# Kernel optimization log

Measured on AMD Instinct MI355X. Metric: run time of the kernel, lower is better.

## Reference

```python
import jax, jax.numpy as jnp
import numpy as np

E = 64          # num_routed_experts
K = 6           # num_experts_per_token
NS = 2          # num_shared_experts
D = 512         # hidden_size
F = 512         # expert_intermediate_size = intermediate_size // 4


def setup_inputs() -> dict:
    key = jax.random.key(0)
    ks = jax.random.split(key, 8)
    s = 0.02
    return {
        "hidden_states": jax.random.normal(ks[0], (2, 1024, D), dtype=jnp.float32),
        "Wr": jax.random.normal(ks[1], (D, E), dtype=jnp.float32) * s,      # router
        "sWg": jax.random.normal(ks[2], (NS, D, F), dtype=jnp.float32) * s,  # shared gate_proj
        "sWu": jax.random.normal(ks[3], (NS, D, F), dtype=jnp.float32) * s,  # shared up_proj
        "sWd": jax.random.normal(ks[4], (NS, F, D), dtype=jnp.float32) * s,  # shared down_proj
        "Wg": jax.random.normal(ks[5], (E, D, F), dtype=jnp.float32) * s,    # routed gate_proj
        "Wu": jax.random.normal(ks[6], (E, D, F), dtype=jnp.float32) * s,    # routed up_proj
        "Wd": jax.random.normal(ks[7], (E, F, D), dtype=jnp.float32) * s,    # routed down_proj
    }


def _swiglu_ffn(x, wg, wu, wd):
    # x: (N, D); wg/wu: (D, F); wd: (F, D)
    return (jax.nn.silu(x @ wg) * (x @ wu)) @ wd


def reference(hidden_states, Wr, sWg, sWu, sWd, Wg, Wu, Wd):
    B, S, d = hidden_states.shape
    x = hidden_states.reshape(-1, d)  # (N, D)
    N = x.shape[0]

    # ---- shared experts (always on) ----
    shared = jnp.zeros_like(x)
    for e in range(NS):
        shared = shared + _swiglu_ffn(x, sWg[e], sWu[e], sWd[e])

    # ---- top-k router ----
    logits = x @ Wr                                   # (N, E)
    probs = jax.nn.softmax(logits, axis=-1)
    top_w, top_i = jax.lax.top_k(probs, K)            # (N, K)
    top_w = top_w / jnp.sum(top_w, axis=-1, keepdims=True)  # renormalize
    gate = jnp.zeros((N, E), dtype=x.dtype).at[jnp.arange(N)[:, None], top_i].set(top_w)

    # ---- routed experts: per-expert FFN, combined with sparse gate ----
    routed = jnp.zeros_like(x)
    for e in range(E):
        routed = routed + _swiglu_ffn(x, Wg[e], Wu[e], Wd[e]) * gate[:, e:e + 1]

    out = (shared + routed + x).reshape(B, S, d)
    return out
```

## Files before the change

kernel.cpp:

```cpp
#include <hip/hip_runtime.h>

#define N_TOK 2048
#define DD 512
#define FF 512
#define EE 64
#define TK 6
#define NG 66
#define RSLOT 12288
#define NSLOT 16384
#define BM 64
#define BN 64

typedef float f32x4 __attribute__((ext_vector_type(4)));
typedef __bf16 bf16x8 __attribute__((ext_vector_type(8)));
typedef short s16x8 __attribute__((ext_vector_type(8)));

__device__ __forceinline__ short f2bf(float f) {
  unsigned u = __builtin_bit_cast(unsigned, f);
  u = (u + 0x7fffu + ((u >> 16) & 1u)) >> 16;
  return (short)u;
}

__global__ void router_k(const float* __restrict__ x, const float* __restrict__ Wr,
                         int* __restrict__ top_i, float* __restrict__ top_w,
                         int* __restrict__ cnt) {
  int wave = threadIdx.x >> 6, lane = threadIdx.x & 63;
  int t0 = (blockIdx.x * 4 + wave) * 4;
  const float* x0 = x + (size_t)t0 * DD;
  float a0 = 0.f, a1 = 0.f, a2 = 0.f, a3 = 0.f;
  for (int k = 0; k < DD; ++k) {
    float wv = Wr[k * EE + lane];
    a0 = fmaf(x0[k], wv, a0);
    a1 = fmaf(x0[DD + k], wv, a1);
    a2 = fmaf(x0[2 * DD + k], wv, a2);
    a3 = fmaf(x0[3 * DD + k], wv, a3);
  }
  float accs[4] = {a0, a1, a2, a3};
#pragma unroll
  for (int tt = 0; tt < 4; ++tt) {
    int t = t0 + tt;
    float acc = accs[tt];
    float m = acc;
#pragma unroll
    for (int s = 32; s; s >>= 1) m = fmaxf(m, __shfl_xor(m, s));
    float p = __expf(acc - m);
    int wi[TK]; float wv[TK];
#pragma unroll
    for (int it = 0; it < TK; ++it) {
      float v = p;
#pragma unroll
      for (int s = 32; s; s >>= 1) v = fmaxf(v, __shfl_xor(v, s));
      unsigned long long b = __ballot(p == v);
      int idx = __ffsll((unsigned long long)b) - 1;
      wi[it] = idx; wv[it] = v;
      if (lane == idx) p = -1.f;
    }
    float wsum = 0.f;
#pragma unroll
    for (int it = 0; it < TK; ++it) wsum += wv[it];
    if (lane < TK) {
      int si = 0; float sv = 0.f;
#pragma unroll
      for (int it = 0; it < TK; ++it) if (lane == it) { si = wi[it]; sv = wv[it]; }
      top_i[t * TK + lane] = si;
      top_w[t * TK + lane] = sv / wsum;
      atomicAdd(&cnt[si], 1);
    }
  }
}

__global__ void offsets_k(const int* __restrict__ cnt, int* __restrict__ goff,
                          int* __restrict__ fill) {
  int i = threadIdx.x;
  if (i < EE) fill[i] = 0;
  if (i == 0) {
    int s = 0;
    for (int e = 0; e < EE; ++e) { goff[e] = s; s += cnt[e]; }
    goff[EE] = RSLOT;
    goff[EE + 1] = RSLOT + N_TOK;
    goff[EE + 2] = RSLOT + 2 * N_TOK;
  }
}

__global__ void scatter_k(const int* __restrict__ top_i, const float* __restrict__ top_w,
                          const int* __restrict__ goff, int* __restrict__ fill,
                          int* __restrict__ btok, float* __restrict__ bw) {
  int idx = blockIdx.x * blockDim.x + threadIdx.x;
  if (idx < RSLOT) {
    int e = top_i[idx];
    int pos = goff[e] + atomicAdd(&fill[e], 1);
    btok[pos] = idx / TK;
    bw[pos] = top_w[idx];
  } else if (idx < NSLOT) {
    int j = idx - RSLOT;
    btok[idx] = j & (N_TOK - 1);
    bw[idx] = 1.0f;
  }
}

__global__ void initout_k(const float* __restrict__ x, float* __restrict__ out, int n4) {
  int i = blockIdx.x * blockDim.x + threadIdx.x;
  if (i < n4) reinterpret_cast<f32x4*>(out)[i] = reinterpret_cast<const f32x4*>(x)[i];
}

__global__ __launch_bounds__(256) void gemm1_k(
    const float* __restrict__ x, const float* __restrict__ Wg, const float* __restrict__ Wu,
    const float* __restrict__ sWg, const float* __restrict__ sWu,
    const int* __restrict__ goff, const int* __restrict__ btok,
    short* __restrict__ H) {
  int g = blockIdx.z;
  int s0g = goff[g], cnt = goff[g + 1] - s0g;
  int mt = blockIdx.y;
  if (mt * BM >= cnt) return;
  int n0 = blockIdx.x * BN;
  const float* wgp = (g < EE) ? Wg + (size_t)g * DD * FF : sWg + (size_t)(g - EE) * DD * FF;
  const float* wup = (g < EE) ? Wu + (size_t)g * DD * FF : sWu + (size_t)(g - EE) * DD * FF;

  __shared__ short laA[4][BM][8];
  __shared__ short lbG[4][BN][8];
  __shared__ short lbU[4][BN][8];

  int tid = threadIdx.x;
  int lane = tid & 63;
  int w = tid >> 6;
  int wr = w >> 1, wc = w & 1;
  int lr = lane & 15, lgq = lane >> 4;

  int sm = tid >> 2, skb = tid & 3;
  int sn = tid & 63, skb2 = tid >> 6;

  int s0 = s0g + mt * BM;
  int tok = btok[((mt * BM + sm) < cnt) ? (s0 + sm) : s0];
  const float* xrow = x + (size_t)tok * DD;

  f32x4 accg[2][2], accu[2][2];
#pragma unroll
  for (int i = 0; i < 2; ++i)
#pragma unroll
    for (int j = 0; j < 2; ++j) {
      accg[i][j] = f32x4{0.f, 0.f, 0.f, 0.f};
      accu[i][j] = f32x4{0.f, 0.f, 0.f, 0.f};
    }

  for (int kt = 0; kt < DD / 32; ++kt) {
    int k0 = kt * 32;
    __syncthreads();
    {
      const float* p = xrow + k0 + skb * 8;
      f32x4 v0 = *reinterpret_cast<const f32x4*>(p);
      f32x4 v1 = *reinterpret_cast<const f32x4*>(p + 4);
      s16x8 o;
      o[0] = f2bf(v0[0]); o[1] = f2bf(v0[1]); o[2] = f2bf(v0[2]); o[3] = f2bf(v0[3]);
      o[4] = f2bf(v1[0]); o[5] = f2bf(v1[1]); o[6] = f2bf(v1[2]); o[7] = f2bf(v1[3]);
      *reinterpret_cast<s16x8*>(&laA[skb][sm][0]) = o;
    }
    {
      const float* bgp = wgp + (size_t)(k0 + skb2 * 8) * FF + n0 + sn;
      const float* bup = wup + (size_t)(k0 + skb2 * 8) * FF + n0 + sn;
      s16x8 og, ou;
#pragma unroll
      for (int i = 0; i < 8; ++i) {
        og[i] = f2bf(bgp[(size_t)i * FF]);
        ou[i] = f2bf(bup[(size_t)i * FF]);
      }
      *reinterpret_cast<s16x8*>(&lbG[skb2][sn][0]) = og;
      *reinterpret_cast<s16x8*>(&lbU[skb2][sn][0]) = ou;
    }
    __syncthreads();
    bf16x8 af[2], bgf[2], buf[2];
#pragma unroll
    for (int i = 0; i < 2; ++i)
      af[i] = *reinterpret_cast<const bf16x8*>(&laA[lgq][wr * 32 + i * 16 + lr][0]);
#pragma unroll
    for (int j = 0; j < 2; ++j) {
      bgf[j] = *reinterpret_cast<const bf16x8*>(&lbG[lgq][wc * 32 + j * 16 + lr][0]);
      buf[j] = *reinterpret_cast<const bf16x8*>(&lbU[lgq][wc * 32 + j * 16 + lr][0]);
    }
#pragma unroll
    for (int i = 0; i < 2; ++i)
#pragma unroll
      for (int j = 0; j < 2; ++j) {
        accg[i][j] = __builtin_amdgcn_mfma_f32_16x16x32_bf16(af[i], bgf[j], accg[i][j], 0, 0, 0);
        accu[i][j] = __builtin_amdgcn_mfma_f32_16x16x32_bf16(af[i], buf[j], accu[i][j], 0, 0, 0);
      }
  }
#pragma unroll
  for (int i = 0; i < 2; ++i)
#pragma unroll
    for (int j = 0; j < 2; ++j)
#pragma unroll
      for (int r = 0; r < 4; ++r) {
        int mrow = wr * 32 + i * 16 + lgq * 4 + r;
        if (mt * BM + mrow < cnt) {
          float gg = accg[i][j][r];
          float uu = accu[i][j][r];
          float hv = (gg / (1.f + __expf(-gg))) * uu;
          int col = n0 + wc * 32 + j * 16 + lr;
          H[(size_t)(s0 + mrow) * FF + col] = f2bf(hv);
        }
      }
}

__global__ __launch_bounds__(256) void gemm2_k(
    const short* __restrict__ H, const float* __restrict__ Wd, const float* __restrict__ sWd,
    const int* __restrict__ goff, const int* __restrict__ btok, const float* __restrict__ bw,
    float* __restrict__ out) {
  int g = blockIdx.z;
  int s0g = goff[g], cnt = goff[g + 1] - s0g;
  int mt = blockIdx.y;
  if (mt * BM >= cnt) return;
  int n0 = blockIdx.x * BN;
  const float* wdp = (g < EE) ? Wd + (size_t)g * FF * DD : sWd + (size_t)(g - EE) * FF * DD;

  __shared__ short laA[4][BM][8];
  __shared__ short lbB[4][BN][8];

  int tid = threadIdx.x;
  int lane = tid & 63;
  int w = tid >> 6;
  int wr = w >> 1, wc = w & 1;
  int lr = lane & 15, lgq = lane >> 4;

  int sm = tid >> 2, skb = tid & 3;
  int sn = tid & 63, skb2 = tid >> 6;

  int s0 = s0g + mt * BM;
  int srow = s0 + sm;
  if (srow > NSLOT - 1) srow = NSLOT - 1;
  const short* hrow = H + (size_t)srow * FF;

  f32x4 acc[2][2];
#pragma unroll
  for (int i = 0; i < 2; ++i)
#pragma unroll
    for (int j = 0; j < 2; ++j) acc[i][j] = f32x4{0.f, 0.f, 0.f, 0.f};

  for (int kt = 0; kt < FF / 32; ++kt) {
    int k0 = kt * 32;
    __syncthreads();
    {
      s16x8 v = *reinterpret_cast<const s16x8*>(hrow + k0 + skb * 8);
      *reinterpret_cast<s16x8*>(&laA[skb][sm][0]) = v;
    }
    {
      const float* bp = wdp + (size_t)(k0 + skb2 * 8) * DD + n0 + sn;
      s16x8 ob;
#pragma unroll
      for (int i = 0; i < 8; ++i) ob[i] = f2bf(bp[(size_t)i * DD]);
      *reinterpret_cast<s16x8*>(&lbB[skb2][sn][0]) = ob;
    }
    __syncthreads();
    bf16x8 af[2], bf[2];
#pragma unroll
    for (int i = 0; i < 2; ++i)
      af[i] = *reinterpret_cast<const bf16x8*>(&laA[lgq][wr * 32 + i * 16 + lr][0]);
#pragma unroll
    for (int j = 0; j < 2; ++j)
      bf[j] = *reinterpret_cast<const bf16x8*>(&lbB[lgq][wc * 32 + j * 16 + lr][0]);
#pragma unroll
    for (int i = 0; i < 2; ++i)
#pragma unroll
      for (int j = 0; j < 2; ++j)
        acc[i][j] = __builtin_amdgcn_mfma_f32_16x16x32_bf16(af[i], bf[j], acc[i][j], 0, 0, 0);
  }
#pragma unroll
  for (int i = 0; i < 2; ++i)
#pragma unroll
    for (int j = 0; j < 2; ++j)
#pragma unroll
      for (int r = 0; r < 4; ++r) {
        int mrow = wr * 32 + i * 16 + lgq * 4 + r;
        if (mt * BM + mrow < cnt) {
          int slot = s0 + mrow;
          int tok = btok[slot];
          float wv = bw[slot];
          int col = n0 + wc * 32 + j * 16 + lr;
          atomicAdd(&out[(size_t)tok * DD + col], acc[i][j][r] * wv);
        }
      }
}

extern "C" void kernel_launch(void* const* d_in, const int* in_sizes, int n_in,
                              void* d_out, int out_size, void* d_ws, size_t ws_size,
                              hipStream_t stream) {
  const float* x   = (const float*)d_in[0];
  const float* Wr  = (const float*)d_in[1];
  const float* sWg = (const float*)d_in[2];
  const float* sWu = (const float*)d_in[3];
  const float* sWd = (const float*)d_in[4];
  const float* Wg  = (const float*)d_in[5];
  const float* Wu  = (const float*)d_in[6];
  const float* Wd  = (const float*)d_in[7];
  float* out = (float*)d_out;

  char* wsb = (char*)d_ws;
  size_t off = 0;
  short* H = (short*)(wsb + off);    off += (size_t)NSLOT * FF * 2;
  int*   top_i = (int*)(wsb + off);  off += (size_t)RSLOT * 4;
  float* top_w = (float*)(wsb + off); off += (size_t)RSLOT * 4;
  int*   btok = (int*)(wsb + off);   off += (size_t)NSLOT * 4;
  float* bwt  = (float*)(wsb + off); off += (size_t)NSLOT * 4;
  int*   cnt  = (int*)(wsb + off);   off += 256;
  int*   fill = (int*)(wsb + off);   off += 256;
  int*   goff = (int*)(wsb + off);   off += 256;

  hipMemsetAsync(cnt, 0, 256, stream);
  router_k<<<N_TOK / 16, 256, 0, stream>>>(x, Wr, top_i, top_w, cnt);
  offsets_k<<<1, 64, 0, stream>>>(cnt, goff, fill);
  scatter_k<<<NSLOT / 256, 256, 0, stream>>>(top_i, top_w, goff, fill, btok, bwt);
  int n4 = out_size / 4;
  initout_k<<<(n4 + 255) / 256, 256, 0, stream>>>(x, out, n4);
  dim3 grid1(FF / BN, N_TOK / BM, NG);
  gemm1_k<<<grid1, 256, 0, stream>>>(x, Wg, Wu, sWg, sWu, goff, btok, H);
  dim3 grid2(DD / BN, N_TOK / BM, NG);
  gemm2_k<<<grid2, 256, 0, stream>>>(H, Wd, sWd, goff, btok, bwt, out);
}
```

Before: 211.3 us.

## Pipeline MoE GEMMs with async global-to-LDS loads and compact tile worklist

Measured after the change: 196.9 us. -6.8%, faster.

```diff
diff --git a/kernel.cpp b/kernel.cpp
--- a/kernel.cpp
+++ b/kernel.cpp
@@ -10,40 +10,75 @@
 #define NSLOT 16384
 #define BM 64
 #define BN 64
+#define NT 16
+#define MAXT 320
 
 typedef float f32x4 __attribute__((ext_vector_type(4)));
 typedef __bf16 bf16x8 __attribute__((ext_vector_type(8)));
-typedef short s16x8 __attribute__((ext_vector_type(8)));
-
-__device__ __forceinline__ short f2bf(float f) {
-  unsigned u = __builtin_bit_cast(unsigned, f);
-  u = (u + 0x7fffu + ((u >> 16) & 1u)) >> 16;
-  return (short)u;
-}
-
-__global__ void router_k(const float* __restrict__ x, const float* __restrict__ Wr,
-                         int* __restrict__ top_i, float* __restrict__ top_w,
-                         int* __restrict__ cnt) {
-  int wave = threadIdx.x >> 6, lane = threadIdx.x & 63;
-  int t0 = (blockIdx.x * 4 + wave) * 4;
-  const float* x0 = x + (size_t)t0 * DD;
-  float a0 = 0.f, a1 = 0.f, a2 = 0.f, a3 = 0.f;
-  for (int k = 0; k < DD; ++k) {
-    float wv = Wr[k * EE + lane];
-    a0 = fmaf(x0[k], wv, a0);
-    a1 = fmaf(x0[DD + k], wv, a1);
-    a2 = fmaf(x0[2 * DD + k], wv, a2);
-    a3 = fmaf(x0[3 * DD + k], wv, a3);
-  }
-  float accs[4] = {a0, a1, a2, a3};
+
+__device__ __forceinline__ unsigned cvtpk(float lo, float hi) {
+  unsigned r;
+  asm("v_cvt_pk_bf16_f32 %0, %1, %2" : "=v"(r) : "v"(lo), "v"(hi));
+  return r;
+}
+
+__device__ __forceinline__ bf16x8 pack8(f32x4 a, f32x4 b) {
+  union { unsigned u[4]; bf16x8 v; } r;
+  r.u[0] = cvtpk(a[0], a[1]); r.u[1] = cvtpk(a[2], a[3]);
+  r.u[2] = cvtpk(b[0], b[1]); r.u[3] = cvtpk(b[2], b[3]);
+  return r.v;
+}
+
+__device__ __forceinline__ void gll16(const void* g, void* l) {
+  __builtin_amdgcn_global_load_lds(
+      (const __attribute__((address_space(1))) unsigned int*)g,
+      (__attribute__((address_space(3))) unsigned int*)l, 16, 0, 0);
+}
+
+__global__ __launch_bounds__(256) void router_k(
+    const float* __restrict__ x, const float* __restrict__ Wr,
+    int* __restrict__ top_i, float* __restrict__ top_w, int* __restrict__ cnt) {
+  __shared__ float xs[16 * 512];
+  __shared__ float part[4][16][64];
+  int tid = threadIdx.x, lane = tid & 63, w = tid >> 6;
+  int t0 = blockIdx.x * 16;
+
+  const f32x4* xin = (const f32x4*)(x + (size_t)t0 * DD);
+  f32x4* xs4 = (f32x4*)xs;
+#pragma unroll
+  for (int i = 0; i < 8; ++i) xs4[i * 256 + tid] = xin[i * 256 + tid];
+  __syncthreads();
+
+  float acc[16];
+#pragma unroll
+  for (int t = 0; t < 16; ++t) acc[t] = 0.f;
+  for (int kk = 0; kk < 32; ++kk) {
+    int k = w * 128 + kk * 4;
+    float w0 = Wr[(size_t)(k + 0) * EE + lane];
+    float w1 = Wr[(size_t)(k + 1) * EE + lane];
+    float w2 = Wr[(size_t)(k + 2) * EE + lane];
+    float w3 = Wr[(size_t)(k + 3) * EE + lane];
+#pragma unroll
+    for (int t = 0; t < 16; ++t) {
+      f32x4 xv = *(const f32x4*)&xs[t * 512 + k];
+      acc[t] = fmaf(xv[0], w0, acc[t]);
+      acc[t] = fmaf(xv[1], w1, acc[t]);
+      acc[t] = fmaf(xv[2], w2, acc[t]);
+      acc[t] = fmaf(xv[3], w3, acc[t]);
+    }
+  }
+#pragma unroll
+  for (int t = 0; t < 16; ++t) part[w][t][lane] = acc[t];
+  __syncthreads();
+
 #pragma unroll
   for (int tt = 0; tt < 4; ++tt) {
-    int t = t0 + tt;
-    float acc = accs[tt];
-    float m = acc;
+    int t = w * 4 + tt;
+    float l0 = part[0][t][lane] + part[1][t][lane] + part[2][t][lane] + part[3][t][lane];
+    float m = l0;
 #pragma unroll
     for (int s = 32; s; s >>= 1) m = fmaxf(m, __shfl_xor(m, s));
-    float p = __expf(acc - m);
+    float p = __expf(l0 - m);
     int wi[TK]; float wv[TK];
 #pragma unroll
     for (int it = 0; it < TK; ++it) {
@@ -58,28 +93,43 @@
     float wsum = 0.f;
 #pragma unroll
     for (int it = 0; it < TK; ++it) wsum += wv[it];
+    int tg = t0 + t;
     if (lane < TK) {
       int si = 0; float sv = 0.f;
 #pragma unroll
       for (int it = 0; it < TK; ++it) if (lane == it) { si = wi[it]; sv = wv[it]; }
-      top_i[t * TK + lane] = si;
-      top_w[t * TK + lane] = sv / wsum;
+      top_i[tg * TK + lane] = si;
+      top_w[tg * TK + lane] = sv / wsum;
       atomicAdd(&cnt[si], 1);
     }
   }
 }
 
 __global__ void offsets_k(const int* __restrict__ cnt, int* __restrict__ goff,
-                          int* __restrict__ fill) {
+                          int* __restrict__ fill, int* __restrict__ wk_g,
+                          int* __restrict__ wk_mt, int* __restrict__ nitems) {
   int i = threadIdx.x;
-  if (i < EE) fill[i] = 0;
-  if (i == 0) {
-    int s = 0;
-    for (int e = 0; e < EE; ++e) { goff[e] = s; s += cnt[e]; }
+  fill[i] = 0;
+  int c = cnt[i];
+  int s = c;
+#pragma unroll
+  for (int d = 1; d < 64; d <<= 1) { int t = __shfl_up(s, d); if (i >= d) s += t; }
+  goff[i] = s - c;
+  if (i == 63) {
     goff[EE] = RSLOT;
     goff[EE + 1] = RSLOT + N_TOK;
     goff[EE + 2] = RSLOT + 2 * N_TOK;
   }
+  int nt = (c + BM - 1) >> 6;
+  int ts = nt;
+#pragma unroll
+  for (int d = 1; d < 64; d <<= 1) { int t = __shfl_up(ts, d); if (i >= d) ts += t; }
+  int texcl = ts - nt;
+  for (int t = 0; t < nt; ++t) { wk_g[texcl + t] = i; wk_mt[texcl + t] = t; }
+  int tot = __shfl(ts, 63);
+  wk_g[tot + i] = EE + (i >> 5);
+  wk_mt[tot + i] = i & 31;
+  if (i == 0) nitems[0] = tot + 64;
 }
 
 __global__ void scatter_k(const int* __restrict__ top_i, const float* __restrict__ top_w,
@@ -107,31 +157,51 @@
     const float* __restrict__ x, const float* __restrict__ Wg, const float* __restrict__ Wu,
     const float* __restrict__ sWg, const float* __restrict__ sWu,
     const int* __restrict__ goff, const int* __restrict__ btok,
+    const int* __restrict__ wk_g, const int* __restrict__ wk_mt,
+    const int* __restrict__ nitems,
     short* __restrict__ H) {
-  int g = blockIdx.z;
+  int item = blockIdx.y;
+  if (item >= nitems[0]) return;
+  int g = wk_g[item], mt = wk_mt[item];
   int s0g = goff[g], cnt = goff[g + 1] - s0g;
-  int mt = blockIdx.y;
-  if (mt * BM >= cnt) return;
   int n0 = blockIdx.x * BN;
   const float* wgp = (g < EE) ? Wg + (size_t)g * DD * FF : sWg + (size_t)(g - EE) * DD * FF;
   const float* wup = (g < EE) ? Wu + (size_t)g * DD * FF : sWu + (size_t)(g - EE) * DD * FF;
 
-  __shared__ short laA[4][BM][8];
-  __shared__ short lbG[4][BN][8];
-  __shared__ short lbU[4][BN][8];
+  __shared__ __align__(16) float lds[2][6144];
 
   int tid = threadIdx.x;
   int lane = tid & 63;
   int w = tid >> 6;
   int wr = w >> 1, wc = w & 1;
   int lr = lane & 15, lgq = lane >> 4;
-
-  int sm = tid >> 2, skb = tid & 3;
-  int sn = tid & 63, skb2 = tid >> 6;
-
   int s0 = s0g + mt * BM;
-  int tok = btok[((mt * BM + sm) < cnt) ? (s0 + sm) : s0];
-  const float* xrow = x + (size_t)tok * DD;
+
+  const float* sp[6];
+  int ldsoff[6], strf[6];
+#pragma unroll
+  for (int q = 0; q < 6; ++q) {
+    int c = w * 6 + q;
+    ldsoff[q] = c * 256;
+    if (c < 8) {
+      int row = c * 8 + (lane >> 3);
+      int tok = btok[s0 + row];
+      sp[q] = x + (size_t)tok * DD + (((lane & 7) ^ (lane >> 3)) << 2);
+      strf[q] = 32;
+    } else if (c < 16) {
+      int cc = c - 8;
+      int krow = cc * 4 + (lane >> 4);
+      int colf = ((((lane & 15) << 4) ^ (((cc >> 1) & 3) << 5)) >> 2);
+      sp[q] = wgp + (size_t)krow * FF + n0 + colf;
+      strf[q] = 32 * FF;
+    } else {
+      int cc = c - 16;
+      int krow = cc * 4 + (lane >> 4);
+      int colf = ((((lane & 15) << 4) ^ (((cc >> 1) & 3) << 5)) >> 2);
+      sp[q] = wup + (size_t)krow * FF + n0 + colf;
+      strf[q] = 32 * FF;
+    }
+  }
 
   f32x4 accg[2][2], accu[2][2];
 #pragma unroll
@@ -142,48 +212,60 @@
       accu[i][j] = f32x4{0.f, 0.f, 0.f, 0.f};
     }
 
-  for (int kt = 0; kt < DD / 32; ++kt) {
-    int k0 = kt * 32;
+  auto STAGE = [&](int b, int kt) {
+#pragma unroll
+    for (int q = 0; q < 6; ++q)
+      gll16(sp[q] + (size_t)kt * strf[q], &lds[b][ldsoff[q]]);
+  };
+  auto COMPUTE = [&](int b) {
+    const float* Am = &lds[b][0];
+    const float* Gm = &lds[b][2048];
+    const float* Um = &lds[b][4096];
+    bf16x8 af[2], bg[2], bu[2];
+#pragma unroll
+    for (int i = 0; i < 2; ++i) {
+      int row = wr * 32 + i * 16 + lr;
+      int sw = (row & 7) << 2;
+      f32x4 v0 = *(const f32x4*)&Am[row * 32 + ((lgq * 8) ^ sw)];
+      f32x4 v1 = *(const f32x4*)&Am[row * 32 + ((lgq * 8 + 4) ^ sw)];
+      af[i] = pack8(v0, v1);
+    }
+#pragma unroll
+    for (int j = 0; j < 2; ++j) {
+      int col = wc * 32 + j * 16 + lr;
+      int cx = col ^ (lgq << 3);
+      int kb = lgq * 8;
+      f32x4 g0, g1, u0, u1;
+#pragma unroll
+      for (int i2 = 0; i2 < 4; ++i2) {
+        g0[i2] = Gm[(kb + i2) * 64 + cx];
+        g1[i2] = Gm[(kb + 4 + i2) * 64 + cx];
+        u0[i2] = Um[(kb + i2) * 64 + cx];
+        u1[i2] = Um[(kb + 4 + i2) * 64 + cx];
+      }
+      bg[j] = pack8(g0, g1);
+      bu[j] = pack8(u0, u1);
+    }
+#pragma unroll
+    for (int i = 0; i < 2; ++i)
+#pragma unroll
+      for (int j = 0; j < 2; ++j) {
+        accg[i][j] = __builtin_amdgcn_mfma_f32_16x16x32_bf16(af[i], bg[j], accg[i][j], 0, 0, 0);
+        accu[i][j] = __builtin_amdgcn_mfma_f32_16x16x32_bf16(af[i], bu[j], accu[i][j], 0, 0, 0);
+      }
+  };
+
+  STAGE(0, 0);
+  __syncthreads();
+  int b = 0;
+#pragma unroll 1
+  for (int kt = 0; kt < NT; ++kt) {
+    if (kt + 1 < NT) STAGE(b ^ 1, kt + 1);
+    COMPUTE(b);
     __syncthreads();
-    {
-      const float* p = xrow + k0 + skb * 8;
-      f32x4 v0 = *reinterpret_cast<const f32x4*>(p);
-      f32x4 v1 = *reinterpret_cast<const f32x4*>(p + 4);
-      s16x8 o;
-      o[0] = f2bf(v0[0]); o[1] = f2bf(v0[1]); o[2] = f2bf(v0[2]); o[3] = f2bf(v0[3]);
-      o[4] = f2bf(v1[0]); o[5] = f2bf(v1[1]); o[6] = f2bf(v1[2]); o[7] = f2bf(v1[3]);
-      *reinterpret_cast<s16x8*>(&laA[skb][sm][0]) = o;
-    }
-    {
-      const float* bgp = wgp + (size_t)(k0 + skb2 * 8) * FF + n0 + sn;
-      const float* bup = wup + (size_t)(k0 + skb2 * 8) * FF + n0 + sn;
-      s16x8 og, ou;
-#pragma unroll
-      for (int i = 0; i < 8; ++i) {
-        og[i] = f2bf(bgp[(size_t)i * FF]);
-        ou[i] = f2bf(bup[(size_t)i * FF]);
-      }
-      *reinterpret_cast<s16x8*>(&lbG[skb2][sn][0]) = og;
-      *reinterpret_cast<s16x8*>(&lbU[skb2][sn][0]) = ou;
-    }
-    __syncthreads();
-    bf16x8 af[2], bgf[2], buf[2];
-#pragma unroll
-    for (int i = 0; i < 2; ++i)
-      af[i] = *reinterpret_cast<const bf16x8*>(&laA[lgq][wr * 32 + i * 16 + lr][0]);
-#pragma unroll
-    for (int j = 0; j < 2; ++j) {
-      bgf[j] = *reinterpret_cast<const bf16x8*>(&lbG[lgq][wc * 32 + j * 16 + lr][0]);
-      buf[j] = *reinterpret_cast<const bf16x8*>(&lbU[lgq][wc * 32 + j * 16 + lr][0]);
-    }
-#pragma unroll
-    for (int i = 0; i < 2; ++i)
-#pragma unroll
-      for (int j = 0; j < 2; ++j) {
-        accg[i][j] = __builtin_amdgcn_mfma_f32_16x16x32_bf16(af[i], bgf[j], accg[i][j], 0, 0, 0);
-        accu[i][j] = __builtin_amdgcn_mfma_f32_16x16x32_bf16(af[i], buf[j], accu[i][j], 0, 0, 0);
-      }
-  }
+    b ^= 1;
+  }
+
 #pragma unroll
   for (int i = 0; i < 2; ++i)
 #pragma unroll
@@ -196,7 +278,7 @@
           float uu = accu[i][j][r];
           float hv = (gg / (1.f + __expf(-gg))) * uu;
           int col = n0 + wc * 32 + j * 16 + lr;
-          H[(size_t)(s0 + mrow) * FF + col] = f2bf(hv);
+          H[(size_t)(s0 + mrow) * FF + col] = (short)(cvtpk(hv, hv) & 0xffffu);
         }
       }
 }
@@ -204,30 +286,44 @@
 __global__ __launch_bounds__(256) void gemm2_k(
     const short* __restrict__ H, const float* __restrict__ Wd, const float* __restrict__ sWd,
     const int* __restrict__ goff, const int* __restrict__ btok, const float* __restrict__ bw,
+    const int* __restrict__ wk_g, const int* __restrict__ wk_mt,
+    const int* __restrict__ nitems,
     float* __restrict__ out) {
-  int g = blockIdx.z;
+  int item = blockIdx.y;
+  if (item >= nitems[0]) return;
+  int g = wk_g[item], mt = wk_mt[item];
   int s0g = goff[g], cnt = goff[g + 1] - s0g;
-  int mt = blockIdx.y;
-  if (mt * BM >= cnt) return;
   int n0 = blockIdx.x * BN;
   const float* wdp = (g < EE) ? Wd + (size_t)g * FF * DD : sWd + (size_t)(g - EE) * FF * DD;
 
-  __shared__ short laA[4][BM][8];
-  __shared__ short lbB[4][BN][8];
+  __shared__ __align__(16) short lds[2][6144];
 
   int tid = threadIdx.x;
   int lane = tid & 63;
   int w = tid >> 6;
   int wr = w >> 1, wc = w & 1;
   int lr = lane & 15, lgq = lane >> 4;
-
-  int sm = tid >> 2, skb = tid & 3;
-  int sn = tid & 63, skb2 = tid >> 6;
-
   int s0 = s0g + mt * BM;
-  int srow = s0 + sm;
-  if (srow > NSLOT - 1) srow = NSLOT - 1;
-  const short* hrow = H + (size_t)srow * FF;
+
+  const char* sp[3];
+  int ldsbyte[3], strb[3];
+#pragma unroll
+  for (int q = 0; q < 3; ++q) {
+    int c = w * 3 + q;
+    ldsbyte[q] = c * 1024;
+    if (c < 4) {
+      int row = c * 16 + (lane >> 2);
+      int slot = s0 + row;
+      sp[q] = (const char*)(H + (size_t)slot * FF + (((lane & 3) ^ ((lane >> 2) & 3)) << 3));
+      strb[q] = 64;
+    } else {
+      int cc = c - 4;
+      int krow = cc * 4 + (lane >> 4);
+      int colf = ((((lane & 15) << 4) ^ (((cc >> 1) & 3) << 5)) >> 2);
+      sp[q] = (const char*)(wdp + (size_t)krow * DD + n0 + colf);
+      strb[q] = 32 * DD * 4;
+    }
+  }
 
   f32x4 acc[2][2];
 #pragma unroll
@@ -235,49 +331,67 @@
 #pragma unroll
     for (int j = 0; j < 2; ++j) acc[i][j] = f32x4{0.f, 0.f, 0.f, 0.f};
 
-  for (int kt = 0; kt < FF / 32; ++kt) {
-    int k0 = kt * 32;
+  auto STAGE = [&](int b, int kt) {
+#pragma unroll
+    for (int q = 0; q < 3; ++q)
+      gll16(sp[q] + (size_t)kt * strb[q], (char*)lds[b] + ldsbyte[q]);
+  };
+  auto COMPUTE = [&](int b) {
+    const short* Hm = lds[b];
+    const float* Bm = (const float*)(lds[b] + 2048);
+    bf16x8 af[2], bd[2];
+#pragma unroll
+    for (int i = 0; i < 2; ++i) {
+      int row = wr * 32 + i * 16 + lr;
+      af[i] = *(const bf16x8*)&Hm[row * 32 + ((lgq * 8) ^ ((row & 3) << 3))];
+    }
+#pragma unroll
+    for (int j = 0; j < 2; ++j) {
+      int col = wc * 32 + j * 16 + lr;
+      int cx = col ^ (lgq << 3);
+      int kb = lgq * 8;
+      f32x4 d0, d1;
+#pragma unroll
+      for (int i2 = 0; i2 < 4; ++i2) {
+        d0[i2] = Bm[(kb + i2) * 64 + cx];
+        d1[i2] = Bm[(kb + 4 + i2) * 64 + cx];
+      }
+      bd[j] = pack8(d0, d1);
+    }
+#pragma unroll
+    for (int i = 0; i < 2; ++i)
+#pragma unroll
+      for (int j = 0; j < 2; ++j)
+        acc[i][j] = __builtin_amdgcn_mfma_f32_16x16x32_bf16(af[i], bd[j], acc[i][j], 0, 0, 0);
+  };
+
+  STAGE(0, 0);
+  __syncthreads();
+  int b = 0;
+#pragma unroll 1
+  for (int kt = 0; kt < NT; ++kt) {
+    if (kt + 1 < NT) STAGE(b ^ 1, kt + 1);
+    COMPUTE(b);
     __syncthreads();
-    {
-      s16x8 v = *reinterpret_cast<const s16x8*>(hrow + k0 + skb * 8);
-      *reinterpret_cast<s16x8*>(&laA[skb][sm][0]) = v;
-    }
-    {
-      const float* bp = wdp + (size_t)(k0 + skb2 * 8) * DD + n0 + sn;
-      s16x8 ob;
-#pragma unroll
-      for (int i = 0; i < 8; ++i) ob[i] = f2bf(bp[(size_t)i * DD]);
-      *reinterpret_cast<s16x8*>(&lbB[skb2][sn][0]) = ob;
-    }
-    __syncthreads();
-    bf16x8 af[2], bf[2];
-#pragma unroll
-    for (int i = 0; i < 2; ++i)
-      af[i] = *reinterpret_cast<const bf16x8*>(&laA[lgq][wr * 32 + i * 16 + lr][0]);
-#pragma unroll
-    for (int j = 0; j < 2; ++j)
-      bf[j] = *reinterpret_cast<const bf16x8*>(&lbB[lgq][wc * 32 + j * 16 + lr][0]);
-#pragma unroll
-    for (int i = 0; i < 2; ++i)
-#pragma unroll
-      for (int j = 0; j < 2; ++j)
-        acc[i][j] = __builtin_amdgcn_mfma_f32_16x16x32_bf16(af[i], bf[j], acc[i][j], 0, 0, 0);
-  }
+    b ^= 1;
+  }
+
 #pragma unroll
   for (int i = 0; i < 2; ++i)
 #pragma unroll
-    for (int j = 0; j < 2; ++j)
-#pragma unroll
-      for (int r = 0; r < 4; ++r) {
-        int mrow = wr * 32 + i * 16 + lgq * 4 + r;
-        if (mt * BM + mrow < cnt) {
-          int slot = s0 + mrow;
-          int tok = btok[slot];
-          float wv = bw[slot];
+    for (int r = 0; r < 4; ++r) {
+      int mrow = wr * 32 + i * 16 + lgq * 4 + r;
+      if (mt * BM + mrow < cnt) {
+        int slot = s0 + mrow;
+        int tok = btok[slot];
+        float wv = bw[slot];
+#pragma unroll
+        for (int j = 0; j < 2; ++j) {
           int col = n0 + wc * 32 + j * 16 + lr;
           atomicAdd(&out[(size_t)tok * DD + col], acc[i][j][r] * wv);
         }
       }
+    }
 }
 
 extern "C" void kernel_launch(void* const* d_in, const int* in_sizes, int n_in,
@@ -295,23 +409,26 @@
 
   char* wsb = (char*)d_ws;
   size_t off = 0;
-  short* H = (short*)(wsb + off);    off += (size_t)NSLOT * FF * 2;
-  int*   top_i = (int*)(wsb + off);  off += (size_t)RSLOT * 4;
+  short* H = (short*)(wsb + off);     off += (size_t)NSLOT * FF * 2;
+  int*   top_i = (int*)(wsb + off);   off += (size_t)RSLOT * 4;
   float* top_w = (float*)(wsb + off); off += (size_t)RSLOT * 4;
-  int*   btok = (int*)(wsb + off);   off += (size_t)NSLOT * 4;
-  float* bwt  = (float*)(wsb + off); off += (size_t)NSLOT * 4;
-  int*   cnt  = (int*)(wsb + off);   off += 256;
-  int*   fill = (int*)(wsb + off);   off += 256;
-  int*   goff = (int*)(wsb + off);   off += 256;
+  int*   btok = (int*)(wsb + off);    off += (size_t)NSLOT * 4;
+  float* bwt  = (float*)(wsb + off);  off += (size_t)NSLOT * 4;
+  int*   cnt  = (int*)(wsb + off);    off += 256;
+  int*   fill = (int*)(wsb + off);    off += 256;
+  int*   goff = (int*)(wsb + off);    off += 512;
+  int*   wk_g = (int*)(wsb + off);    off += MAXT * 4;
+  int*   wk_mt = (int*)(wsb + off);   off += MAXT * 4;
+  int*   nitems = (int*)(wsb + off);  off += 256;
 
   hipMemsetAsync(cnt, 0, 256, stream);
   router_k<<<N_TOK / 16, 256, 0, stream>>>(x, Wr, top_i, top_w, cnt);
-  offsets_k<<<1, 64, 0, stream>>>(cnt, goff, fill);
+  offsets_k<<<1, 64, 0, stream>>>(cnt, goff, fill, wk_g, wk_mt, nitems);
   scatter_k<<<NSLOT / 256, 256, 0, stream>>>(top_i, top_w, goff, fill, btok, bwt);
   int n4 = out_size / 4;
   initout_k<<<(n4 + 255) / 256, 256, 0, stream>>>(x, out, n4);
-  dim3 grid1(FF / BN, N_TOK / BM, NG);
-  gemm1_k<<<grid1, 256, 0, stream>>>(x, Wg, Wu, sWg, sWu, goff, btok, H);
-  dim3 grid2(DD / BN, N_TOK / BM, NG);
-  gemm2_k<<<grid2, 256, 0, stream>>>(H, Wd, sWd, goff, btok, bwt, out);
-}
+  dim3 grid1(FF / BN, MAXT, 1);
+  gemm1_k<<<grid1, 256, 0, stream>>>(x, Wg, Wu, sWg, sWu, goff, btok, wk_g, wk_mt, nitems, H);
+  dim3 grid2(DD / BN, MAXT, 1);
+  gemm2_k<<<grid2, 256, 0, stream>>>(H, Wd, sWd, goff, btok, bwt, wk_g, wk_mt, nitems, out);
+}
```
